# Optimization experiments

Hardware: AMD Instinct MI355X
Metric: run time of the kernel (lower is better)

The kernel has to match this reference:

```python
import jax, jax.numpy as jnp
import numpy as np

B, NB, C, T = 8, 1024, 1024, 32
NUM_HEADS = 4
HEAD_DIM = max((C // 1) // NUM_HEADS, 1)  # reduce_ratio = 1
D = HEAD_DIM * NUM_HEADS                   # 1024
WIN = 9
DILATION = 1


def setup_inputs() -> dict:
    key = jax.random.key(0)
    ks = jax.random.split(key, 6)
    std = 0.02
    return {
        "xb": jax.random.normal(ks[0], (B, NB, C, T), dtype=jnp.float32),
        "Wq": jax.random.normal(ks[1], (C, D), dtype=jnp.float32) * std,
        "Wk": jax.random.normal(ks[2], (C, D), dtype=jnp.float32) * std,
        "Wv": jax.random.normal(ks[3], (C, D), dtype=jnp.float32) * std,
        "Wo": jax.random.normal(ks[4], (D, C), dtype=jnp.float32) * std,
        "pos": jax.random.normal(ks[5], (NB, D), dtype=jnp.float32) * std,
    }


def _neighbor_index(nb, win, dilation):
    # [NB, W] clamped sliding-window indices (static, built with numpy)
    half = (win - 1) // 2
    offs = np.arange(-half, half + 1) * dilation
    idx = np.arange(nb)[:, None] + offs[None, :]
    return np.clip(idx, 0, nb - 1)


def reference(xb, Wq, Wk, Wv, Wo, pos):
    # xb: [B, NB, C, T]
    tokens = xb.mean(axis=-1)                    # [B, NB, C]
    Q = tokens @ Wq + pos                        # [B, NB, D]
    K = tokens @ Wk + pos
    V = tokens @ Wv + pos

    nbr = _neighbor_index(xb.shape[1], WIN, DILATION)  # [NB, W]
    Kn = K[:, nbr]                               # [B, NB, W, D] direct gather
    Vn = V[:, nbr]                               # [B, NB, W, D]

    scale = 1.0 / jnp.sqrt(jnp.asarray(D, dtype=Q.dtype))
    scores = jnp.einsum('bnd,bnwd->bnw', Q, Kn) * scale
    attn = jax.nn.softmax(scores, axis=-1)       # [B, NB, W]
    ctx = jnp.einsum('bnw,bnwd->bnd', attn, Vn)  # [B, NB, D]
    out_tok = ctx @ Wo                           # [B, NB, C]
    return xb + out_tok[..., None]               # broadcast over T, residual
```

## Files before the change

kernel.cpp:

```cpp
#include <hip/hip_runtime.h>

typedef __bf16 bf16x8 __attribute__((ext_vector_type(8)));
typedef float  f32x4  __attribute__((ext_vector_type(4)));

#define B_    8
#define NB_   1024
#define C_    1024
#define T_    32
#define D_    1024
#define M_    (B_ * NB_)
#define N3_   (3 * D_)
#define WIN_  9
#define HALF_ 4

__device__ __forceinline__ void gload_lds16(const void* g, void* l) {
    __builtin_amdgcn_global_load_lds(
        (const __attribute__((address_space(1))) void*)(unsigned long long)(uintptr_t)g,
        (__attribute__((address_space(3))) void*)(unsigned int)(uintptr_t)l,
        16, 0, 0);
}

__global__ __launch_bounds__(256) void mean_kernel(const float* __restrict__ xb,
                                                   __bf16* __restrict__ tok) {
    int gid  = blockIdx.x * 256 + threadIdx.x;
    int wave = gid >> 6;
    int lane = gid & 63;
    int o     = (wave << 3) + (lane >> 3);
    int chunk = lane & 7;
    const float4* p = (const float4*)(xb + (size_t)o * T_ + chunk * 4);
    float4 v = *p;
    float s = v.x + v.y + v.z + v.w;
    s += __shfl_xor(s, 1);
    s += __shfl_xor(s, 2);
    s += __shfl_xor(s, 4);
    if (chunk == 0) tok[o] = (__bf16)(s * (1.0f / 32.0f));
}

__global__ __launch_bounds__(256) void transpose_kernel(
    const float* __restrict__ Wq, const float* __restrict__ Wk,
    const float* __restrict__ Wv, const float* __restrict__ Wo,
    __bf16* __restrict__ Wqkvt, __bf16* __restrict__ Wot) {
    __shared__ float tile[32][33];
    int mat = blockIdx.z;
    const float* src = (mat == 0) ? Wq : (mat == 1) ? Wk : (mat == 2) ? Wv : Wo;
    __bf16* dst = (mat < 3) ? (Wqkvt + (size_t)mat * 1024 * 1024) : Wot;
    int tx = threadIdx.x, ty = threadIdx.y;
    int x  = blockIdx.x * 32 + tx;
    int y0 = blockIdx.y * 32;
#pragma unroll
    for (int j = 0; j < 32; j += 8)
        tile[ty + j][tx] = src[(size_t)(y0 + ty + j) * 1024 + x];
    __syncthreads();
    int k = y0 + tx;
#pragma unroll
    for (int j = 0; j < 32; j += 8) {
        int n = blockIdx.x * 32 + ty + j;
        dst[(size_t)n * 1024 + k] = (__bf16)tile[tx][ty + j];
    }
}

template <int MODE>
__global__ __launch_bounds__(256) void gemm_kernel(
    const __bf16* __restrict__ A, const __bf16* __restrict__ Bt,
    int K, int Ncols,
    const float* __restrict__ pos, __bf16* __restrict__ Cbf,
    float* __restrict__ corr) {
    constexpr int BM = 128, BK = 32;
    __shared__ __align__(16) __bf16 As[BM * BK];
    __shared__ __align__(16) __bf16 Bs[BM * BK];
    int tid = threadIdx.x;
    int wid = tid >> 6, lane = tid & 63;
    int wr = wid >> 1, wc = wid & 1;
    int l15 = lane & 15, lg = lane >> 4;
    int row0 = blockIdx.x * BM, col0 = blockIdx.y * BM;

    int srow = lane >> 2;
    int scol = (lane & 3) * 8;

    f32x4 acc[4][4] = {};

    for (int kt = 0; kt < K; kt += BK) {
#pragma unroll
        for (int i = 0; i < 2; i++) {
            int s = wid + i * 4;
            gload_lds16(A  + (size_t)(row0 + s * 16 + srow) * K + kt + scol, &As[s * 512]);
            gload_lds16(Bt + (size_t)(col0 + s * 16 + srow) * K + kt + scol, &Bs[s * 512]);
        }
        __syncthreads();
        bf16x8 fa[4], fb[4];
#pragma unroll
        for (int m = 0; m < 4; m++)
            fa[m] = *(const bf16x8*)&As[(wr * 64 + m * 16 + l15) * BK + lg * 8];
#pragma unroll
        for (int n = 0; n < 4; n++)
            fb[n] = *(const bf16x8*)&Bs[(wc * 64 + n * 16 + l15) * BK + lg * 8];
#pragma unroll
        for (int m = 0; m < 4; m++)
#pragma unroll
            for (int n = 0; n < 4; n++)
                acc[m][n] = __builtin_amdgcn_mfma_f32_16x16x32_bf16(fa[m], fb[n], acc[m][n], 0, 0, 0);
        __syncthreads();
    }

#pragma unroll
    for (int m = 0; m < 4; m++) {
#pragma unroll
        for (int n = 0; n < 4; n++) {
            int col = col0 + wc * 64 + n * 16 + l15;
#pragma unroll
            for (int r = 0; r < 4; r++) {
                int row = row0 + wr * 64 + m * 16 + lg * 4 + r;
                float v = acc[m][n][r];
                if (MODE == 0) {
                    v += pos[((row & 1023) << 10) + (col & 1023)];
                    Cbf[(size_t)row * Ncols + col] = (__bf16)v;
                } else {
                    corr[(size_t)row * 1024 + col] = v;
                }
            }
        }
    }
}

__global__ __launch_bounds__(256) void attn_kernel(const __bf16* __restrict__ QKV,
                                                   __bf16* __restrict__ ctx) {
    int wg   = blockIdx.x * 4 + (threadIdx.x >> 6);
    int lane = threadIdx.x & 63;
    int n = wg & 1023;
    int browbase = wg - n;

    const __bf16* qrow = QKV + (size_t)wg * N3_;
    bf16x8 q0 = *(const bf16x8*)(qrow + lane * 8);
    bf16x8 q1 = *(const bf16x8*)(qrow + 512 + lane * 8);
    float qf[16];
#pragma unroll
    for (int i = 0; i < 8; i++) { qf[i] = (float)q0[i]; qf[8 + i] = (float)q1[i]; }

    float sc[WIN_];
#pragma unroll
    for (int w = 0; w < WIN_; w++) {
        int nn = n - HALF_ + w;
        nn = (nn < 0) ? 0 : (nn > 1023 ? 1023 : nn);
        const __bf16* krow = QKV + (size_t)(browbase + nn) * N3_ + D_;
        bf16x8 k0 = *(const bf16x8*)(krow + lane * 8);
        bf16x8 k1 = *(const bf16x8*)(krow + 512 + lane * 8);
        float s = 0.f;
#pragma unroll
        for (int i = 0; i < 8; i++)
            s += qf[i] * (float)k0[i] + qf[8 + i] * (float)k1[i];
        s += __shfl_xor(s, 32); s += __shfl_xor(s, 16); s += __shfl_xor(s, 8);
        s += __shfl_xor(s, 4);  s += __shfl_xor(s, 2);  s += __shfl_xor(s, 1);
        sc[w] = s * 0.03125f;
    }

    float mx = sc[0];
#pragma unroll
    for (int w = 1; w < WIN_; w++) mx = fmaxf(mx, sc[w]);
    float e[WIN_], sum = 0.f;
#pragma unroll
    for (int w = 0; w < WIN_; w++) { e[w] = __expf(sc[w] - mx); sum += e[w]; }
    float inv = 1.0f / sum;

    float accv[16];
#pragma unroll
    for (int i = 0; i < 16; i++) accv[i] = 0.f;
#pragma unroll
    for (int w = 0; w < WIN_; w++) {
        int nn = n - HALF_ + w;
        nn = (nn < 0) ? 0 : (nn > 1023 ? 1023 : nn);
        const __bf16* vrow = QKV + (size_t)(browbase + nn) * N3_ + 2 * D_;
        bf16x8 v0 = *(const bf16x8*)(vrow + lane * 8);
        bf16x8 v1 = *(const bf16x8*)(vrow + 512 + lane * 8);
        float aw = e[w] * inv;
#pragma unroll
        for (int i = 0; i < 8; i++) {
            accv[i]     += aw * (float)v0[i];
            accv[8 + i] += aw * (float)v1[i];
        }
    }

    bf16x8 o0, o1;
#pragma unroll
    for (int i = 0; i < 8; i++) { o0[i] = (__bf16)accv[i]; o1[i] = (__bf16)accv[8 + i]; }
    __bf16* crow = ctx + (size_t)wg * D_;
    *(bf16x8*)(crow + lane * 8) = o0;
    *(bf16x8*)(crow + 512 + lane * 8) = o1;
}

__global__ __launch_bounds__(256) void add_kernel(const float* __restrict__ xb,
                                                  const float* __restrict__ corr,
                                                  float* __restrict__ outp) {
    const long long total4 = (long long)M_ * C_ * T_ / 4;
    long long stride = (long long)gridDim.x * 256;
    for (long long i = (long long)blockIdx.x * 256 + threadIdx.x; i < total4; i += stride) {
        float c = corr[i >> 3];
        const float4* xp = (const float4*)xb + i;
        float4 x = *xp;
        x.x += c; x.y += c; x.z += c; x.w += c;
        ((float4*)outp)[i] = x;
    }
}

extern "C" void kernel_launch(void* const* d_in, const int* in_sizes, int n_in,
                              void* d_out, int out_size, void* d_ws, size_t ws_size,
                              hipStream_t stream) {
    const float* xb  = (const float*)d_in[0];
    const float* Wq  = (const float*)d_in[1];
    const float* Wk  = (const float*)d_in[2];
    const float* Wv  = (const float*)d_in[3];
    const float* Wo  = (const float*)d_in[4];
    const float* pos = (const float*)d_in[5];
    float* out = (float*)d_out;

    char* ws = (char*)d_ws;
    __bf16* tokens = (__bf16*)(ws);
    __bf16* wqkvt  = (__bf16*)(ws + 16777216);
    __bf16* wot    = (__bf16*)(ws + 23068672);
    __bf16* qkv    = (__bf16*)(ws + 25165824);
    __bf16* ctx    = (__bf16*)(ws + 75497472);
    float*  corr   = (float*)(ws + 25165824);

    mean_kernel<<<dim3((M_ * C_) / 32), dim3(256), 0, stream>>>(xb, tokens);

    transpose_kernel<<<dim3(32, 32, 4), dim3(32, 8), 0, stream>>>(Wq, Wk, Wv, Wo, wqkvt, wot);

    gemm_kernel<0><<<dim3(M_ / 128, N3_ / 128), dim3(256), 0, stream>>>(
        tokens, wqkvt, 1024, N3_, pos, qkv, nullptr);

    attn_kernel<<<dim3(M_ / 4), dim3(256), 0, stream>>>(qkv, ctx);

    gemm_kernel<1><<<dim3(M_ / 128, C_ / 128), dim3(256), 0, stream>>>(
        ctx, wot, 1024, C_, nullptr, nullptr, corr);

    add_kernel<<<dim3(4096), dim3(256), 0, stream>>>(xb, corr, out);
}
```

Before: 830.9 us.

## Triple-buffer GEMM loads, swizzle workgroups, use nontemporal streaming in mean/add

The GEMM kernel now prefetches k-tiles two steps ahead into a 3-slot LDS ring, with explicit vmcnt waits and one barrier per step, so global loads overlap with MFMA work. Workgroup IDs are remapped across XCDs through a 1D grid to improve L2 locality of shared tiles. The mean and add kernels use nontemporal loads and stores on the large streaming tensor to avoid cache pollution, and the add loop is unrolled. This uses triple the LDS per block, which may reduce occupancy, and it hardcodes the tile count and the K loop length.

Result: faster. 804.7 us (-3.2%).

```diff
diff --git a/kernel.cpp b/kernel.cpp
--- a/kernel.cpp
+++ b/kernel.cpp
@@ -27,8 +27,8 @@
     int lane = gid & 63;
     int o     = (wave << 3) + (lane >> 3);
     int chunk = lane & 7;
-    const float4* p = (const float4*)(xb + (size_t)o * T_ + chunk * 4);
-    float4 v = *p;
+    const f32x4* p = (const f32x4*)(xb + (size_t)o * T_ + chunk * 4);
+    f32x4 v = __builtin_nontemporal_load(p);
     float s = v.x + v.y + v.z + v.w;
     s += __shfl_xor(s, 1);
     s += __shfl_xor(s, 2);
@@ -65,41 +65,55 @@
     int K, int Ncols,
     const float* __restrict__ pos, __bf16* __restrict__ Cbf,
     float* __restrict__ corr) {
-    constexpr int BM = 128, BK = 32;
-    __shared__ __align__(16) __bf16 As[BM * BK];
-    __shared__ __align__(16) __bf16 Bs[BM * BK];
+    constexpr int BM = 128, BK = 32, KT = 32;
+    __shared__ __align__(16) __bf16 As[3][BM * BK];
+    __shared__ __align__(16) __bf16 Bs[3][BM * BK];
     int tid = threadIdx.x;
     int wid = tid >> 6, lane = tid & 63;
     int wr = wid >> 1, wc = wid & 1;
     int l15 = lane & 15, lg = lane >> 4;
-    int row0 = blockIdx.x * BM, col0 = blockIdx.y * BM;
+
+    int q = gridDim.x >> 3;
+    int wg = (blockIdx.x & 7) * q + (blockIdx.x >> 3);
+    int row0 = (wg & 63) * BM;
+    int col0 = (wg >> 6) * BM;
 
     int srow = lane >> 2;
     int scol = (lane & 3) * 8;
 
     f32x4 acc[4][4] = {};
 
-    for (int kt = 0; kt < K; kt += BK) {
+    auto STAGE = [&](int t, int slot) {
 #pragma unroll
         for (int i = 0; i < 2; i++) {
             int s = wid + i * 4;
-            gload_lds16(A  + (size_t)(row0 + s * 16 + srow) * K + kt + scol, &As[s * 512]);
-            gload_lds16(Bt + (size_t)(col0 + s * 16 + srow) * K + kt + scol, &Bs[s * 512]);
+            gload_lds16(A  + (size_t)(row0 + s * 16 + srow) * K + t * BK + scol, &As[slot][s * 512]);
+            gload_lds16(Bt + (size_t)(col0 + s * 16 + srow) * K + t * BK + scol, &Bs[slot][s * 512]);
         }
-        __syncthreads();
+    };
+
+    STAGE(0, 0);
+    STAGE(1, 1);
+
+    for (int t = 0; t < KT; ++t) {
+        int slot = t % 3;
+        if (t == KT - 1) asm volatile("s_waitcnt vmcnt(0)" ::: "memory");
+        else             asm volatile("s_waitcnt vmcnt(4)" ::: "memory");
+        __builtin_amdgcn_s_barrier();
+        __builtin_amdgcn_sched_barrier(0);
+        if (t + 2 < KT) STAGE(t + 2, (t + 2) % 3);
         bf16x8 fa[4], fb[4];
 #pragma unroll
         for (int m = 0; m < 4; m++)
-            fa[m] = *(const bf16x8*)&As[(wr * 64 + m * 16 + l15) * BK + lg * 8];
+            fa[m] = *(const bf16x8*)&As[slot][(wr * 64 + m * 16 + l15) * BK + lg * 8];
 #pragma unroll
         for (int n = 0; n < 4; n++)
-            fb[n] = *(const bf16x8*)&Bs[(wc * 64 + n * 16 + l15) * BK + lg * 8];
+            fb[n] = *(const bf16x8*)&Bs[slot][(wc * 64 + n * 16 + l15) * BK + lg * 8];
 #pragma unroll
         for (int m = 0; m < 4; m++)
 #pragma unroll
             for (int n = 0; n < 4; n++)
                 acc[m][n] = __builtin_amdgcn_mfma_f32_16x16x32_bf16(fa[m], fb[n], acc[m][n], 0, 0, 0);
-        __syncthreads();
     }
 
 #pragma unroll
@@ -192,12 +206,12 @@
                                                   float* __restrict__ outp) {
     const long long total4 = (long long)M_ * C_ * T_ / 4;
     long long stride = (long long)gridDim.x * 256;
+#pragma unroll 4
     for (long long i = (long long)blockIdx.x * 256 + threadIdx.x; i < total4; i += stride) {
         float c = corr[i >> 3];
-        const float4* xp = (const float4*)xb + i;
-        float4 x = *xp;
+        f32x4 x = __builtin_nontemporal_load((const f32x4*)xb + i);
         x.x += c; x.y += c; x.z += c; x.w += c;
-        ((float4*)outp)[i] = x;
+        __builtin_nontemporal_store(x, (f32x4*)outp + i);
     }
 }
 
@@ -224,12 +238,12 @@
 
     transpose_kernel<<<dim3(32, 32, 4), dim3(32, 8), 0, stream>>>(Wq, Wk, Wv, Wo, wqkvt, wot);
 
-    gemm_kernel<0><<<dim3(M_ / 128, N3_ / 128), dim3(256), 0, stream>>>(
+    gemm_kernel<0><<<dim3(1536), dim3(256), 0, stream>>>(
         tokens, wqkvt, 1024, N3_, pos, qkv, nullptr);
 
     attn_kernel<<<dim3(M_ / 4), dim3(256), 0, stream>>>(qkv, ctx);
 
-    gemm_kernel<1><<<dim3(M_ / 128, C_ / 128), dim3(256), 0, stream>>>(
+    gemm_kernel<1><<<dim3(512), dim3(256), 0, stream>>>(
         ctx, wot, 1024, C_, nullptr, nullptr, corr);
 
     add_kernel<<<dim3(4096), dim3(256), 0, stream>>>(xb, corr, out);
```
